# Kernel tuning notes

Measured on AMD Instinct MI355X. Metric: run time of the kernel, lower is better.

## Reference

```python
import jax, jax.numpy as jnp
import numpy as np

B, T, D = 8, 2048, 1024
NUM_HEADS = 16
SCALE = 1.0 / np.sqrt(D // NUM_HEADS).astype(np.float32)  # sqrt(d_modal//num_heads), per source


def setup_inputs() -> dict:
    key = jax.random.key(0)
    ks = jax.random.split(key, 7)
    s = 1.0 / np.sqrt(D).astype(np.float32)
    return {
        "x": jax.random.normal(ks[0], (B, T, D), dtype=jnp.float32),
        "Wq_w": jax.random.normal(ks[1], (D, D), dtype=jnp.float32) * s,
        "Wq_b": jax.random.normal(ks[2], (D,), dtype=jnp.float32) * 0.01,
        "Wk_w": jax.random.normal(ks[3], (D, D), dtype=jnp.float32) * s,
        "Wk_b": jax.random.normal(ks[4], (D,), dtype=jnp.float32) * 0.01,
        "Wv_w": jax.random.normal(ks[5], (D, D), dtype=jnp.float32) * s,
        "Wv_b": jax.random.normal(ks[6], (D,), dtype=jnp.float32) * 0.01,
    }


def reference(x, Wq_w, Wq_b, Wk_w, Wk_b, Wv_w, Wv_b):
    # Linear projections (torch nn.Linear: y = x @ W.T + b)
    Q = jnp.einsum('btd,ed->bte', x, Wq_w) + Wq_b
    K = jnp.einsum('btd,ed->bte', x, Wk_w) + Wk_b
    V = jnp.einsum('btd,ed->bte', x, Wv_w) + Wv_b
    # scores [B, T, T], scaled by 1/sqrt(d_modal // num_heads) as in source
    scores = jnp.einsum('bqd,bkd->bqk', Q, K) * SCALE
    causal = jnp.tril(jnp.ones((T, T), dtype=bool))  # tril mask buffer
    scores = jnp.where(causal, scores, -jnp.inf)
    attn = jax.nn.softmax(scores, axis=-1)
    return jnp.einsum('bqk,bkd->bqd', attn, V)
```

## Files before the change

kernel.cpp:

```cpp
#include <hip/hip_runtime.h>


typedef float f32x4 __attribute__((ext_vector_type(4)));
typedef _Float16 half8 __attribute__((ext_vector_type(8)));
typedef _Float16 half4 __attribute__((ext_vector_type(4)));

#define DEVINL __device__ __forceinline__
static constexpr float ATT_SCALE = 0.125f;

DEVINL void gload_lds16(const _Float16* g, _Float16* l) {
  __builtin_amdgcn_global_load_lds((const __attribute__((address_space(1))) void*)g,
                                   (__attribute__((address_space(3))) void*)l, 16, 0, 0);
}

#define SBAR() __builtin_amdgcn_sched_barrier(0)

#define MM(AOFF, BOFF, ASET, BSET) \
  _Pragma("unroll") for (int kk_ = 0; kk_ < 2; ++kk_) \
  _Pragma("unroll") for (int i_ = 0; i_ < 4; ++i_) \
  _Pragma("unroll") for (int jj_ = 0; jj_ < 2; ++jj_) \
    acc[(AOFF) + i_][(BOFF) + jj_] = __builtin_amdgcn_mfma_f32_16x16x32_f16( \
        ASET[i_][kk_], BSET[jj_][kk_], acc[(AOFF) + i_][(BOFF) + jj_], 0, 0, 0);
#define PH_BAR() SBAR(); __builtin_amdgcn_s_barrier(); \
    __builtin_amdgcn_s_setprio(1)
#define PH_DONE() __builtin_amdgcn_s_setprio(0); SBAR()

template <int LDA, int LDB, class GA, class GB>
DEVINL void gemm_core(GA ga, GB gb, int NT, char* ldsb, int tid, f32x4 acc[8][4]) {
  const int l = tid & 63, w = tid >> 6;
  const int wm = w >> 2, wn = w & 3;
  const int lr = l & 15, lk = l >> 4;
  int srow[2], scol[2];
#pragma unroll
  for (int i = 0; i < 2; ++i) {
    const int P = i * 512 + w * 64 + l;
    srow[i] = P >> 3;
    scol[i] = (P & 7) ^ (srow[i] & 7);
  }
  const int ch0 = ((lk ^ (lr & 7)) << 4);
  const int ch1 = (((lk + 4) ^ (lr & 7)) << 4);
  const int abase = lr * 128;
  const int bbase = (wn & 1) * 8192 + lr * 128;

  half8 aA[4][2], aB[4][2], bA[2][2], bB[2][2];

  auto STGA = [&](int t, int h, int bufb) {
    const _Float16* g0 = ga(t, h);
    char* dst = ldsb + bufb * 65536 + h * 16384;
#pragma unroll
    for (int i = 0; i < 2; ++i)
      gload_lds16(g0 + (size_t)srow[i] * LDA + scol[i] * 8,
                  (_Float16*)(dst + i * 8192 + w * 1024));
  };
  auto STGB = [&](int t, int h, int bufb) {
    const _Float16* g0 = gb(t, h);
    char* dst = ldsb + bufb * 65536 + 32768 + h * 16384;
#pragma unroll
    for (int i = 0; i < 2; ++i)
      gload_lds16(g0 + (size_t)srow[i] * LDB + scol[i] * 8,
                  (_Float16*)(dst + i * 8192 + w * 1024));
  };
  auto RDA = [&](int bufb, int ih, half8 d[4][2]) {
    const char* sA = ldsb + bufb * 65536 + wm * 16384 + ih * 8192;
#pragma unroll
    for (int i = 0; i < 4; ++i) {
      d[i][0] = *(const half8*)(sA + abase + i * 2048 + ch0);
      d[i][1] = *(const half8*)(sA + abase + i * 2048 + ch1);
    }
  };
  auto RDB = [&](int bufb, int jh, half8 d[2][2]) {
    const char* sB = ldsb + bufb * 65536 + 32768 + (wn >> 1) * 16384 + jh * 4096;
#pragma unroll
    for (int jj = 0; jj < 2; ++jj) {
      d[jj][0] = *(const half8*)(sB + bbase + jj * 2048 + ch0);
      d[jj][1] = *(const half8*)(sB + bbase + jj * 2048 + ch1);
    }
  };

  auto tile = [&](int t, bool stA, bool stB) {
    const int bufb = t & 1, obuf = bufb ^ 1;
    RDB(bufb, 1, bB);
    if (stA) STGA(t + 1, 0, obuf);
    PH_BAR(); MM(0, 0, aA, bA); PH_DONE();
    RDA(bufb, 1, aB);
    if (stA) STGA(t + 1, 1, obuf);
    PH_BAR(); MM(0, 2, aA, bB); PH_DONE();
    if (stB) STGB(t + 2, 0, bufb);
    SBAR();
    if (stB)      { asm volatile("s_waitcnt vmcnt(2)" ::: "memory"); }
    else if (stA) { asm volatile("s_waitcnt vmcnt(0)" ::: "memory"); }
    PH_BAR(); MM(4, 0, aB, bA); PH_DONE();
    if (stA) { RDA(obuf, 0, aA); RDB(obuf, 0, bA); }
    if (stB) STGB(t + 2, 1, bufb);
    PH_BAR(); MM(4, 2, aB, bB); PH_DONE();
  };

  STGA(0, 0, 0); STGA(0, 1, 0); STGB(0, 0, 0); STGB(0, 1, 0);
  STGB(1, 0, 1); STGB(1, 1, 1);
  asm volatile("s_waitcnt vmcnt(4)" ::: "memory");
  __builtin_amdgcn_s_barrier(); SBAR();
  RDA(0, 0, aA); RDB(0, 0, bA);
  for (int t = 0; t < NT - 2; ++t) tile(t, true, true);
  tile(NT - 2, true, false);
  tile(NT - 1, false, false);
}

template <int LDA, int LDB, class GA, class GB>
DEVINL void gemm_n128(GA ga, GB gb, int NT, char* ldsb, int tid, f32x4 acc[4][4]) {
  const int l = tid & 63, w = tid >> 6;
  const int wm = w >> 1, wn = w & 1;
  const int lr = l & 15, lk = l >> 4;
  int srow[2], scol[2];
#pragma unroll
  for (int i = 0; i < 2; ++i) {
    const int P = i * 512 + w * 64 + l;
    srow[i] = P >> 3;
    scol[i] = (P & 7) ^ (srow[i] & 7);
  }
  const int ch0 = ((lk ^ (lr & 7)) << 4);
  const int ch1 = (((lk + 4) ^ (lr & 7)) << 4);
  const int abase = (wm >> 1) * 16384 + ((wm & 1) * 64 + lr) * 128;
  const int bbase = 32768 + (wn * 64 + lr) * 128;

  auto STG = [&](const _Float16* g0, int ld, int bufb, int slot) {
    char* dst = ldsb + bufb * 49152 + slot * 16384;
#pragma unroll
    for (int i = 0; i < 2; ++i)
      gload_lds16(g0 + (size_t)srow[i] * ld + scol[i] * 8,
                  (_Float16*)(dst + i * 8192 + w * 1024));
  };
  half8 a[4][2], bfr[4][2];
  auto RD = [&](int bufb) {
    const char* bb = ldsb + bufb * 49152;
#pragma unroll
    for (int i = 0; i < 4; ++i) {
      a[i][0] = *(const half8*)(bb + abase + i * 2048 + ch0);
      a[i][1] = *(const half8*)(bb + abase + i * 2048 + ch1);
    }
#pragma unroll
    for (int j = 0; j < 4; ++j) {
      bfr[j][0] = *(const half8*)(bb + bbase + j * 2048 + ch0);
      bfr[j][1] = *(const half8*)(bb + bbase + j * 2048 + ch1);
    }
  };

  STG(ga(0, 0), LDA, 0, 0); STG(ga(0, 1), LDA, 0, 1); STG(gb(0), LDB, 0, 2);
  STG(ga(1, 0), LDA, 1, 0); STG(ga(1, 1), LDA, 1, 1); STG(gb(1), LDB, 1, 2);
  asm volatile("s_waitcnt vmcnt(6)" ::: "memory");
  __builtin_amdgcn_s_barrier();

  for (int t = 0; t < NT; ++t) {
    const int bufb = t & 1;
    RD(bufb);
    SBAR();
    __builtin_amdgcn_s_barrier();
    asm volatile("s_waitcnt lgkmcnt(0)" ::: "memory");
    SBAR();
    __builtin_amdgcn_s_setprio(1);
#pragma unroll
    for (int i = 0; i < 4; ++i)
#pragma unroll
      for (int j = 0; j < 4; ++j)
        acc[i][j] = __builtin_amdgcn_mfma_f32_16x16x32_f16(a[i][0], bfr[j][0], acc[i][j], 0, 0, 0);
    __builtin_amdgcn_s_setprio(0);
    SBAR();
    __builtin_amdgcn_s_barrier();
    if (t + 2 < NT) {
      STG(ga(t + 2, 0), LDA, bufb, 0);
      STG(ga(t + 2, 1), LDA, bufb, 1);
      STG(gb(t + 2), LDB, bufb, 2);
      asm volatile("s_waitcnt vmcnt(6)" ::: "memory");
    } else if (t + 1 < NT) {
      asm volatile("s_waitcnt vmcnt(0)" ::: "memory");
    }
    SBAR();
    __builtin_amdgcn_s_barrier();
    __builtin_amdgcn_s_setprio(1);
#pragma unroll
    for (int i = 0; i < 4; ++i)
#pragma unroll
      for (int j = 0; j < 4; ++j)
        acc[i][j] = __builtin_amdgcn_mfma_f32_16x16x32_f16(a[i][1], bfr[j][1], acc[i][j], 0, 0, 0);
    __builtin_amdgcn_s_setprio(0);
    SBAR();
    __builtin_amdgcn_s_barrier();
  }
}

__global__ __launch_bounds__(256) void cvt_all(const float* __restrict__ x,
                                               const float* __restrict__ wq,
                                               const float* __restrict__ wk,
                                               const float* __restrict__ wv,
                                               _Float16* __restrict__ xh,
                                               _Float16* __restrict__ wqh,
                                               _Float16* __restrict__ wkh,
                                               _Float16* __restrict__ wvh) {
  const int n8 = 2490368;
  for (int i = blockIdx.x * 256 + threadIdx.x; i < n8; i += 2048 * 256) {
    const float* src; _Float16* dst; int off;
    if (i < 2097152)      { src = x;  dst = xh;  off = i; }
    else if (i < 2228224) { src = wq; dst = wqh; off = i - 2097152; }
    else if (i < 2359296) { src = wk; dst = wkh; off = i - 2228224; }
    else                  { src = wv; dst = wvh; off = i - 2359296; }
    const float4* p = (const float4*)src + (size_t)off * 2;
    float4 v0 = p[0], v1 = p[1];
    half8 h;
    h[0] = (_Float16)v0.x; h[1] = (_Float16)v0.y; h[2] = (_Float16)v0.z; h[3] = (_Float16)v0.w;
    h[4] = (_Float16)v1.x; h[5] = (_Float16)v1.y; h[6] = (_Float16)v1.z; h[7] = (_Float16)v1.w;
    *((half8*)dst + off) = h;
  }
}

__global__ __launch_bounds__(512) void gemm_qkv(
    const _Float16* __restrict__ xh, const _Float16* __restrict__ Wqh,
    const _Float16* __restrict__ Wkh, const _Float16* __restrict__ Wvh,
    const float* __restrict__ bq, const float* __restrict__ bk,
    const float* __restrict__ bv, _Float16* __restrict__ Qh,
    _Float16* __restrict__ Kh, _Float16* __restrict__ VT) {
  __shared__ _Float16 lds[65536];
  const int tid = threadIdx.x;
  const int bid = blockIdx.x;
  const int swz = (bid & 7) * 96 + (bid >> 3);
  const int mt = swz / 12, nt = swz % 12;
  const int sel = nt >> 2;
  const _Float16* Wsel = sel == 0 ? Wqh : (sel == 1 ? Wkh : Wvh);
  const float* bsel = sel == 0 ? bq : (sel == 1 ? bk : bv);
  const _Float16* Ab = xh + (size_t)mt * 256 * 1024;
  const _Float16* Bb = Wsel + (size_t)(nt & 3) * 256 * 1024;
  f32x4 acc[8][4] = {};
  auto ga = [&](int t, int h) { return Ab + (size_t)h * 128 * 1024 + t * 64; };
  auto gb = [&](int t, int h) { return Bb + (size_t)h * 128 * 1024 + t * 64; };
  gemm_core<1024, 1024>(ga, gb, 16, (char*)lds, tid, acc);
  const int l = tid & 63, w = tid >> 6;
  const int wm = w >> 2, wn = w & 3;
  const int lr = l & 15, lk = l >> 4;
  const int n0 = (nt & 3) * 256;
  __syncthreads();
#pragma unroll
  for (int ai = 0; ai < 8; ++ai) {
    const int rbase = wm * 128 + (ai >> 2) * 64 + (ai & 3) * 16 + lk * 4;
#pragma unroll
    for (int j = 0; j < 4; ++j) {
      const int col = wn * 64 + j * 16 + lr;
      const float bvv = bsel[n0 + col];
#pragma unroll
      for (int r = 0; r < 4; ++r) {
        const int row = rbase + r;
        const float v = acc[ai][j][r] + bvv;
        if (sel < 2)
          lds[row * 256 + ((col + (row >> 2) * 16) & 255)] = (_Float16)v;
        else
          lds[col * 256 + ((row + (col >> 2) * 16) & 255)] = (_Float16)v;
      }
    }
  }
  __syncthreads();
#pragma unroll
  for (int i = 0; i < 16; ++i) {
    const int c = i * 512 + tid;
    const int row = c >> 5, c8 = c & 31;
    half8 v = *(const half8*)&lds[row * 256 + ((c8 * 8 + (row >> 2) * 16) & 255)];
    if (sel < 2) {
      _Float16* Out = sel == 0 ? Qh : Kh;
      *(half8*)&Out[(size_t)(mt * 256 + row) * 1024 + n0 + c8 * 8] = v;
    } else {
      const int bb = mt >> 3, t0 = (mt & 7) * 256;
      *(half8*)&VT[((size_t)bb * 1024 + n0 + row) * 2048 + t0 + c8 * 8] = v;
    }
  }
}

__global__ __launch_bounds__(512) void gemm_qk(const _Float16* __restrict__ Qh,
                                               const _Float16* __restrict__ Kh,
                                               _Float16* __restrict__ Sc) {
  __shared__ _Float16 lds[49152];
  const int tid = threadIdx.x;
  const int j = blockIdx.x;
  const int b = j / 72, r = j % 72;
  int qt = 0, cum = 0;
  while (cum + (qt + 1) * 2 <= r) { cum += (qt + 1) * 2; ++qt; }
  const int jn = r - cum;
  const _Float16* Ab = Qh + ((size_t)b * 2048 + qt * 256) * 1024;
  const _Float16* Bb = Kh + ((size_t)b * 2048 + jn * 128) * 1024;
  f32x4 acc[4][4] = {};
  auto ga = [&](int t, int h) { return Ab + (size_t)h * 128 * 1024 + t * 64; };
  auto gb = [&](int t) { return Bb + t * 64; };
  gemm_n128<1024, 1024>(ga, gb, 16, (char*)lds, tid, acc);
  const int l = tid & 63, w = tid >> 6;
  const int wm = w >> 1, wn = w & 1;
  const int lr = l & 15, lk = l >> 4;
  _Float16* St = Sc + ((size_t)b * 36 + (size_t)(qt * (qt + 1) / 2) + (jn >> 1)) * 65536 +
                 (jn & 1) * 128;
  const _Float16 NINF = (_Float16)(-__builtin_inff());
#pragma unroll
  for (int i = 0; i < 4; ++i) {
#pragma unroll
    for (int jj = 0; jj < 4; ++jj) {
      const int col = wn * 64 + jj * 16 + lr;
      const int kg = jn * 128 + col;
#pragma unroll
      for (int rr = 0; rr < 4; ++rr) {
        const int row = wm * 64 + i * 16 + lk * 4 + rr;
        const int qg = qt * 256 + row;
        St[(size_t)row * 256 + col] =
            (kg <= qg) ? (_Float16)(acc[i][jj][rr] * ATT_SCALE) : NINF;
      }
    }
  }
}

__global__ __launch_bounds__(256) void softmax_p(const _Float16* __restrict__ Sc,
                                                 _Float16* __restrict__ Pc) {
  const int l = threadIdx.x & 63;
  const int gid = blockIdx.x * 4 + (threadIdx.x >> 6);
  const int b = gid >> 11, q = gid & 2047;
  const int qt = q >> 8, rq = q & 255;
  const int ntile = qt + 1;
  const size_t base = ((size_t)b * 36 + (size_t)(qt * (qt + 1) / 2)) * 65536 +
                      (size_t)rq * 256 + l * 4;
  float vx[32];
  float m = -__builtin_inff();
#pragma unroll
  for (int c = 0; c < 8; ++c) {
    float x0 = -__builtin_inff(), x1 = x0, x2 = x0, x3 = x0;
    if (c < ntile) {
      half4 t = *(const half4*)&Sc[base + (size_t)c * 65536];
      x0 = (float)t[0]; x1 = (float)t[1]; x2 = (float)t[2]; x3 = (float)t[3];
    }
    vx[4 * c] = x0; vx[4 * c + 1] = x1; vx[4 * c + 2] = x2; vx[4 * c + 3] = x3;
    m = fmaxf(m, fmaxf(fmaxf(x0, x1), fmaxf(x2, x3)));
  }
#pragma unroll
  for (int s = 1; s < 64; s <<= 1) m = fmaxf(m, __shfl_xor(m, s, 64));
  float sum = 0.f;
#pragma unroll
  for (int i = 0; i < 32; ++i) { vx[i] = __expf(vx[i] - m); sum += vx[i]; }
#pragma unroll
  for (int s = 1; s < 64; s <<= 1) sum += __shfl_xor(sum, s, 64);
  const float inv = 1.f / sum;
  _Float16* Pb = Pc + base;
#pragma unroll
  for (int c = 0; c < 8; ++c) {
    if (c < ntile) {
      half4 p;
      p[0] = (_Float16)(vx[4 * c] * inv);
      p[1] = (_Float16)(vx[4 * c + 1] * inv);
      p[2] = (_Float16)(vx[4 * c + 2] * inv);
      p[3] = (_Float16)(vx[4 * c + 3] * inv);
      *(half4*)&Pb[(size_t)c * 65536] = p;
    }
  }
}

__global__ __launch_bounds__(512) void gemm_pv(const _Float16* __restrict__ Pc,
                                               const _Float16* __restrict__ VT,
                                               float* __restrict__ O) {
  __shared__ _Float16 lds[49152];
  const int tid = threadIdx.x;
  const int j = blockIdx.x;
  const int qt = 7 - (j >> 6);
  const int dt = (j >> 3) & 7, b = j & 7;
  const _Float16* Pb = Pc + ((size_t)b * 36 + (size_t)(qt * (qt + 1) / 2)) * 65536;
  const _Float16* Vb = VT + ((size_t)b * 1024 + dt * 128) * 2048;
  f32x4 acc[4][4] = {};
  auto ga = [&](int t, int h) {
    return Pb + (size_t)(t >> 2) * 65536 + (size_t)h * 32768 + (t & 3) * 64;
  };
  auto gb = [&](int t) { return Vb + t * 64; };
  gemm_n128<256, 2048>(ga, gb, (qt + 1) * 4, (char*)lds, tid, acc);
  const int l = tid & 63, w = tid >> 6;
  const int wm = w >> 1, wn = w & 1;
  const int lr = l & 15, lk = l >> 4;
#pragma unroll
  for (int i = 0; i < 4; ++i) {
#pragma unroll
    for (int jj = 0; jj < 4; ++jj) {
      const int cg = dt * 128 + wn * 64 + jj * 16 + lr;
#pragma unroll
      for (int rr = 0; rr < 4; ++rr) {
        const int rg = qt * 256 + wm * 64 + i * 16 + lk * 4 + rr;
        O[((size_t)b * 2048 + rg) * 1024 + cg] = acc[i][jj][rr];
      }
    }
  }
}

extern "C" void kernel_launch(void* const* d_in, const int* in_sizes, int n_in,
                              void* d_out, int out_size, void* d_ws, size_t ws_size,
                              hipStream_t stream) {
  const float* x    = (const float*)d_in[0];
  const float* Wq_w = (const float*)d_in[1];
  const float* Wq_b = (const float*)d_in[2];
  const float* Wk_w = (const float*)d_in[3];
  const float* Wk_b = (const float*)d_in[4];
  const float* Wv_w = (const float*)d_in[5];
  const float* Wv_b = (const float*)d_in[6];
  float* out = (float*)d_out;
  char* ws = (char*)d_ws;
  _Float16* xh  = (_Float16*)(ws);
  _Float16* Wqh = (_Float16*)(ws + 33554432);
  _Float16* Wkh = (_Float16*)(ws + 35651584);
  _Float16* Wvh = (_Float16*)(ws + 37748736);
  _Float16* Sc  = (_Float16*)(ws);
  _Float16* Qh  = (_Float16*)(ws + 75497472);
  _Float16* Kh  = (_Float16*)(ws + 109051904);
  _Float16* Pc  = (_Float16*)(ws + 75497472);
  _Float16* VT  = (_Float16*)(ws + 142606336);

  cvt_all<<<2048, 256, 0, stream>>>(x, Wq_w, Wk_w, Wv_w, xh, Wqh, Wkh, Wvh);
  gemm_qkv<<<768, 512, 0, stream>>>(xh, Wqh, Wkh, Wvh, Wq_b, Wk_b, Wv_b, Qh, Kh, VT);
  gemm_qk<<<576, 512, 0, stream>>>(Qh, Kh, Sc);
  softmax_p<<<4096, 256, 0, stream>>>(Sc, Pc);
  gemm_pv<<<512, 512, 0, stream>>>(Pc, VT, out);
}
```

Before: 275.4 us.

## Restructure QKV projection GEMM mainloop into two barrier phases per k-tile

Replaces the four-phase ping-pong GEMM mainloop, which had four barriers per k-tile, with a two-phase schedule for the QKV projection kernel. The full B fragment for the warp is read into registers once per tile, the first half of the MFMAs runs, then the second half, with fewer barriers and larger global-to-LDS stage batches. The aim is to cut barrier and scheduling overhead, at the cost of more live registers (bC holds 8 fragments) and coarser overlap of loads with compute.

Result: no change. 274.0 us (-0.5%).

```diff
diff --git a/kernel.cpp b/kernel.cpp
--- a/kernel.cpp
+++ b/kernel.cpp
@@ -15,18 +15,8 @@
 
 #define SBAR() __builtin_amdgcn_sched_barrier(0)
 
-#define MM(AOFF, BOFF, ASET, BSET) \
-  _Pragma("unroll") for (int kk_ = 0; kk_ < 2; ++kk_) \
-  _Pragma("unroll") for (int i_ = 0; i_ < 4; ++i_) \
-  _Pragma("unroll") for (int jj_ = 0; jj_ < 2; ++jj_) \
-    acc[(AOFF) + i_][(BOFF) + jj_] = __builtin_amdgcn_mfma_f32_16x16x32_f16( \
-        ASET[i_][kk_], BSET[jj_][kk_], acc[(AOFF) + i_][(BOFF) + jj_], 0, 0, 0);
-#define PH_BAR() SBAR(); __builtin_amdgcn_s_barrier(); \
-    __builtin_amdgcn_s_setprio(1)
-#define PH_DONE() __builtin_amdgcn_s_setprio(0); SBAR()
-
 template <int LDA, int LDB, class GA, class GB>
-DEVINL void gemm_core(GA ga, GB gb, int NT, char* ldsb, int tid, f32x4 acc[8][4]) {
+DEVINL void gemm_2ph(GA ga, GB gb, int NT, char* ldsb, int tid, f32x4 acc[8][4]) {
   const int l = tid & 63, w = tid >> 6;
   const int wm = w >> 2, wn = w & 3;
   const int lr = l & 15, lk = l >> 4;
@@ -40,26 +30,31 @@
   const int ch0 = ((lk ^ (lr & 7)) << 4);
   const int ch1 = (((lk + 4) ^ (lr & 7)) << 4);
   const int abase = lr * 128;
-  const int bbase = (wn & 1) * 8192 + lr * 128;
-
-  half8 aA[4][2], aB[4][2], bA[2][2], bB[2][2];
-
-  auto STGA = [&](int t, int h, int bufb) {
-    const _Float16* g0 = ga(t, h);
-    char* dst = ldsb + bufb * 65536 + h * 16384;
-#pragma unroll
-    for (int i = 0; i < 2; ++i)
-      gload_lds16(g0 + (size_t)srow[i] * LDA + scol[i] * 8,
-                  (_Float16*)(dst + i * 8192 + w * 1024));
-  };
-  auto STGB = [&](int t, int h, int bufb) {
-    const _Float16* g0 = gb(t, h);
-    char* dst = ldsb + bufb * 65536 + 32768 + h * 16384;
-#pragma unroll
-    for (int i = 0; i < 2; ++i)
-      gload_lds16(g0 + (size_t)srow[i] * LDB + scol[i] * 8,
-                  (_Float16*)(dst + i * 8192 + w * 1024));
-  };
+  const int bbase = (wn >> 1) * 16384 + (wn & 1) * 8192 + lr * 128;
+
+  auto STGA = [&](int t, int bufb) {
+#pragma unroll
+    for (int h = 0; h < 2; ++h) {
+      const _Float16* g0 = ga(t, h);
+      char* dst = ldsb + bufb * 65536 + h * 16384;
+#pragma unroll
+      for (int i = 0; i < 2; ++i)
+        gload_lds16(g0 + (size_t)srow[i] * LDA + scol[i] * 8,
+                    (_Float16*)(dst + i * 8192 + w * 1024));
+    }
+  };
+  auto STGB = [&](int t, int bufb) {
+#pragma unroll
+    for (int h = 0; h < 2; ++h) {
+      const _Float16* g0 = gb(t, h);
+      char* dst = ldsb + bufb * 65536 + 32768 + h * 16384;
+#pragma unroll
+      for (int i = 0; i < 2; ++i)
+        gload_lds16(g0 + (size_t)srow[i] * LDB + scol[i] * 8,
+                    (_Float16*)(dst + i * 8192 + w * 1024));
+    }
+  };
+  half8 aA[4][2], aB[4][2], bC[4][2];
   auto RDA = [&](int bufb, int ih, half8 d[4][2]) {
     const char* sA = ldsb + bufb * 65536 + wm * 16384 + ih * 8192;
 #pragma unroll
@@ -68,41 +63,56 @@
       d[i][1] = *(const half8*)(sA + abase + i * 2048 + ch1);
     }
   };
-  auto RDB = [&](int bufb, int jh, half8 d[2][2]) {
-    const char* sB = ldsb + bufb * 65536 + 32768 + (wn >> 1) * 16384 + jh * 4096;
-#pragma unroll
-    for (int jj = 0; jj < 2; ++jj) {
-      d[jj][0] = *(const half8*)(sB + bbase + jj * 2048 + ch0);
-      d[jj][1] = *(const half8*)(sB + bbase + jj * 2048 + ch1);
-    }
-  };
-
-  auto tile = [&](int t, bool stA, bool stB) {
-    const int bufb = t & 1, obuf = bufb ^ 1;
-    RDB(bufb, 1, bB);
-    if (stA) STGA(t + 1, 0, obuf);
-    PH_BAR(); MM(0, 0, aA, bA); PH_DONE();
-    RDA(bufb, 1, aB);
-    if (stA) STGA(t + 1, 1, obuf);
-    PH_BAR(); MM(0, 2, aA, bB); PH_DONE();
-    if (stB) STGB(t + 2, 0, bufb);
-    SBAR();
-    if (stB)      { asm volatile("s_waitcnt vmcnt(2)" ::: "memory"); }
-    else if (stA) { asm volatile("s_waitcnt vmcnt(0)" ::: "memory"); }
-    PH_BAR(); MM(4, 0, aB, bA); PH_DONE();
-    if (stA) { RDA(obuf, 0, aA); RDB(obuf, 0, bA); }
-    if (stB) STGB(t + 2, 1, bufb);
-    PH_BAR(); MM(4, 2, aB, bB); PH_DONE();
-  };
-
-  STGA(0, 0, 0); STGA(0, 1, 0); STGB(0, 0, 0); STGB(0, 1, 0);
-  STGB(1, 0, 1); STGB(1, 1, 1);
+  auto RDB8 = [&](int bufb) {
+    const char* sB = ldsb + bufb * 65536 + 32768;
+#pragma unroll
+    for (int j = 0; j < 4; ++j) {
+      bC[j][0] = *(const half8*)(sB + bbase + j * 2048 + ch0);
+      bC[j][1] = *(const half8*)(sB + bbase + j * 2048 + ch1);
+    }
+  };
+
+#define MMQ() _Pragma("unroll") for (int kk_ = 0; kk_ < 2; ++kk_) \
+    _Pragma("unroll") for (int i_ = 0; i_ < 4; ++i_) \
+    _Pragma("unroll") for (int j_ = 0; j_ < 4; ++j_) \
+      acc[i_][j_] = __builtin_amdgcn_mfma_f32_16x16x32_f16( \
+          aA[i_][kk_], bC[j_][kk_], acc[i_][j_], 0, 0, 0);
+#define MMH(JO) _Pragma("unroll") for (int kk_ = 0; kk_ < 2; ++kk_) \
+    _Pragma("unroll") for (int i_ = 0; i_ < 4; ++i_) \
+    _Pragma("unroll") for (int jj_ = 0; jj_ < 2; ++jj_) \
+      acc[4 + i_][(JO) + jj_] = __builtin_amdgcn_mfma_f32_16x16x32_f16( \
+          aB[i_][kk_], bC[(JO) + jj_][kk_], acc[4 + i_][(JO) + jj_], 0, 0, 0);
+
+  STGA(0, 0); STGB(0, 0); STGB(1, 1);
   asm volatile("s_waitcnt vmcnt(4)" ::: "memory");
   __builtin_amdgcn_s_barrier(); SBAR();
-  RDA(0, 0, aA); RDB(0, 0, bA);
-  for (int t = 0; t < NT - 2; ++t) tile(t, true, true);
-  tile(NT - 2, true, false);
-  tile(NT - 1, false, false);
+  RDA(0, 0, aA);
+
+  for (int t = 0; t < NT; ++t) {
+    const int bufb = t & 1, obuf = bufb ^ 1;
+    RDB8(bufb);
+    RDA(bufb, 1, aB);
+    if (t + 1 < NT) STGA(t + 1, obuf);
+    SBAR(); __builtin_amdgcn_s_barrier();
+    __builtin_amdgcn_s_setprio(1);
+    MMQ();
+    __builtin_amdgcn_s_setprio(0); SBAR();
+    if (t + 2 < NT) {
+      STGB(t + 2, bufb);
+      asm volatile("s_waitcnt vmcnt(4)" ::: "memory");
+    } else {
+      asm volatile("s_waitcnt vmcnt(0)" ::: "memory");
+    }
+    SBAR(); __builtin_amdgcn_s_barrier();
+    __builtin_amdgcn_s_setprio(1);
+    MMH(0);
+    MMH(2);
+    __builtin_amdgcn_s_setprio(0);
+    if (t + 1 < NT) RDA(obuf, 0, aA);
+    SBAR();
+  }
+#undef MMQ
+#undef MMH
 }
 
 template <int LDA, int LDB, class GA, class GB>
@@ -230,7 +240,7 @@
   f32x4 acc[8][4] = {};
   auto ga = [&](int t, int h) { return Ab + (size_t)h * 128 * 1024 + t * 64; };
   auto gb = [&](int t, int h) { return Bb + (size_t)h * 128 * 1024 + t * 64; };
-  gemm_core<1024, 1024>(ga, gb, 16, (char*)lds, tid, acc);
+  gemm_2ph<1024, 1024>(ga, gb, 16, (char*)lds, tid, acc);
   const int l = tid & 63, w = tid >> 6;
   const int wm = w >> 2, wn = w & 3;
   const int lr = l & 15, lk = l >> 4;
```
